# Optimization experiments

Hardware: AMD Instinct MI355X
Metric: run time of the kernel (lower is better)

The kernel has to match this reference:

```python
import jax, jax.numpy as jnp
import numpy as np

NUM_HEADS = 16


def setup_inputs() -> dict:
    key = jax.random.key(0)
    k1, k2, k3 = jax.random.split(key, 3)
    B, N, C = 8, 1024, 1024
    x = jax.random.normal(k1, (B, N, C), dtype=jnp.float32)
    w_qkv = jax.random.normal(k2, (3 * C, C), dtype=jnp.float32) * (C ** -0.5)
    w_proj = jax.random.normal(k3, (C, C), dtype=jnp.float32) * (C ** -0.5)
    b_proj = jnp.zeros((C,), dtype=jnp.float32)
    return {"x": x, "w_qkv": w_qkv, "w_proj": w_proj, "b_proj": b_proj}


def reference(x, w_qkv, w_proj, b_proj):
    B, N, C = x.shape
    H = NUM_HEADS
    d = C // H
    scale = d ** -0.5
    # qkv projection: (B, N, 3C) -> (3, B, H, N, d)
    qkv = jnp.einsum('bnc,oc->bno', x, w_qkv)
    qkv = qkv.reshape(B, N, 3, H, d).transpose(2, 0, 3, 1, 4)
    q, k, v = qkv[0], qkv[1], qkv[2]
    # spatial attention
    attn = jnp.einsum('bhnd,bhmd->bhnm', q, k) * scale
    attn = jax.nn.softmax(attn, axis=-1)
    out = jnp.einsum('bhnm,bhmd->bhnd', attn, v)
    out = out.transpose(0, 2, 1, 3).reshape(B, N, C)
    # output projection
    return jnp.einsum('bnc,oc->bno', out, w_proj) + b_proj
```

## Files before the change

### kernel.cpp

```cpp
#include <hip/hip_runtime.h>
#include <hip/hip_bf16.h>

typedef unsigned short u16;
typedef unsigned int u32;
typedef __bf16 bf16x8 __attribute__((ext_vector_type(8)));
typedef float f32x4 __attribute__((ext_vector_type(4)));

__device__ __forceinline__ u16 f2b(float f) {
    __bf16 h = (__bf16)f;
    return __builtin_bit_cast(u16, h);
}
__device__ __forceinline__ u32 f2b2(float lo, float hi) {
    return (u32)f2b(lo) | ((u32)f2b(hi) << 16);
}
__device__ __forceinline__ f32x4 mfma16(bf16x8 a, bf16x8 b, f32x4 c) {
    return __builtin_amdgcn_mfma_f32_16x16x32_bf16(a, b, c, 0, 0, 0);
}
__device__ __forceinline__ void async16(const u16* gsrc, u16* ldst) {
    __builtin_amdgcn_global_load_lds(
        (const __attribute__((address_space(1))) void*)gsrc,
        (__attribute__((address_space(3))) void*)ldst, 16, 0, 0);
}
__device__ __forceinline__ float exp2_raw(float x) {
#if __has_builtin(__builtin_amdgcn_exp2f)
    return __builtin_amdgcn_exp2f(x);
#else
    float r; asm("v_exp_f32 %0, %1" : "=v"(r) : "v"(x)); return r;
#endif
}

__global__ __launch_bounds__(256) void cvt_all(const float* __restrict__ x,
                                               const float* __restrict__ wq,
                                               const float* __restrict__ wp,
                                               u16* __restrict__ xb,
                                               u16* __restrict__ wqb,
                                               u16* __restrict__ wpb) {
    int i = (blockIdx.x * 256 + threadIdx.x) * 4;
    const float* src; u16* dst; int off; float scl;
    if (i < 8388608)       { src = x;  dst = xb;  off = i;            scl = 1.f; }
    else if (i < 9437184)  { src = wq; dst = wqb; off = i - 8388608;  scl = 0.18033688f; }
    else if (i < 11534336) { src = wq; dst = wqb; off = i - 8388608;  scl = 1.f; }
    else                   { src = wp; dst = wpb; off = i - 11534336; scl = 1.f; }
    float4 f = *(const float4*)(src + off);
    ushort4 o;
    o.x = f2b(f.x * scl); o.y = f2b(f.y * scl);
    o.z = f2b(f.z * scl); o.w = f2b(f.w * scl);
    *(ushort4*)(dst + off) = o;
}

template <bool F32OUT>
__device__ __forceinline__ void gemm_core(const u16* __restrict__ A,
                                          const u16* __restrict__ B,
                                          void* __restrict__ Cptr,
                                          const float* __restrict__ bias,
                                          int N, int K, int bm, int bn,
                                          u16* As, u16* Bs) {
    const int tid  = threadIdx.x;
    const int lane = tid & 63, wid = tid >> 6;
    const int quad = lane >> 4, l16 = lane & 15;
    const int wm = (wid >> 1) * 64, wn = (wid & 1) * 64;
    const int swr = l16 & 7;

    const int srow8  = lane >> 3;
    const int schunk = ((lane & 7) ^ srow8) << 3;

    const u16* Abase = A + (size_t)(bm * 128) * K;
    const u16* Bbase = B + (size_t)(bn * 128) * K;

    f32x4 acc[4][4] = {};

    for (int k0 = 0; k0 < K; k0 += 64) {
        __syncthreads();
#pragma unroll
        for (int j = 0; j < 4; ++j) {
            int rg = wid * 32 + j * 8;
            async16(Abase + (size_t)(rg + srow8) * K + k0 + schunk, &As[rg * 64]);
            async16(Bbase + (size_t)(rg + srow8) * K + k0 + schunk, &Bs[rg * 64]);
        }
        __syncthreads();
#pragma unroll
        for (int s = 0; s < 2; ++s) {
            bf16x8 af[4], bfr[4];
#pragma unroll
            for (int mt = 0; mt < 4; mt++) {
                int r = wm + mt * 16 + l16;
                af[mt] = *(const bf16x8*)&As[r * 64 + (((s * 4 + quad) ^ swr) << 3)];
            }
#pragma unroll
            for (int nt = 0; nt < 4; nt++) {
                int r = wn + nt * 16 + l16;
                bfr[nt] = *(const bf16x8*)&Bs[r * 64 + (((s * 4 + quad) ^ swr) << 3)];
            }
#pragma unroll
            for (int mt = 0; mt < 4; mt++)
#pragma unroll
                for (int nt = 0; nt < 4; nt++)
                    acc[mt][nt] = mfma16(af[mt], bfr[nt], acc[mt][nt]);
        }
    }
#pragma unroll
    for (int mt = 0; mt < 4; mt++) {
#pragma unroll
        for (int nt = 0; nt < 4; nt++) {
            int row = bm * 128 + wm + mt * 16 + quad * 4;
            int col = bn * 128 + wn + nt * 16 + l16;
            float bv = F32OUT ? bias[col] : 0.f;
#pragma unroll
            for (int r = 0; r < 4; r++) {
                if (F32OUT)
                    ((float*)Cptr)[(size_t)(row + r) * N + col] = acc[mt][nt][r] + bv;
                else
                    ((u16*)Cptr)[(size_t)(row + r) * N + col] = f2b(acc[mt][nt][r]);
            }
        }
    }
}

__global__ __launch_bounds__(256) void gemm_qkvt(const u16* __restrict__ xb,
                                                 const u16* __restrict__ wqkvb,
                                                 u16* __restrict__ qkb,
                                                 u16* __restrict__ vTb) {
    __shared__ u16 As[128 * 64];
    __shared__ u16 Bs[128 * 64];
    int id = blockIdx.x;
    if (id < 1024) {
        gemm_core<false>(xb, wqkvb, qkb, nullptr, 2048, 1024, id >> 4, id & 15, As, Bs);
    } else {
        int t = id - 1024;
        gemm_core<false>(wqkvb + (size_t)2048 * 1024, xb, vTb, nullptr,
                         8192, 1024, t >> 6, t & 63, As, Bs);
    }
}

__global__ __launch_bounds__(256) void gemm_proj(const u16* __restrict__ A,
                                                 const u16* __restrict__ B,
                                                 void* __restrict__ C,
                                                 const float* __restrict__ bias) {
    __shared__ u16 As[128 * 64];
    __shared__ u16 Bs[128 * 64];
    gemm_core<true>(A, B, C, bias, 1024, 1024, blockIdx.y, blockIdx.x, As, Bs);
}

__global__ __launch_bounds__(256, 5) void attn_kernel(const u16* __restrict__ qk,
                                                      const u16* __restrict__ vT,
                                                      u16* __restrict__ outb) {
    __shared__ u16 Ks[64 * 64];
    __shared__ u16 Vt[2][64 * 64];
    __shared__ u16 Ps[4 * 16 * 64];
    const int tid = threadIdx.x, lane = tid & 63, wid = tid >> 6;
    const int quad = lane >> 4, l16 = lane & 15;
    const int p = blockIdx.x;
    const int slot = p >> 3;
    const int bh = (p & 7) * 16 + (slot >> 4);
    const int qt = slot & 15;
    const int b = bh >> 4, h = bh & 15;
    const size_t base = (size_t)b * 1024;
    const int hoff = h * 64;

    const int sr_ = lane >> 3;
    const int sc_ = ((lane & 7) ^ sr_) * 8;
    const int sw = l16 & 7;

    const u16* qptr = qk + (base + qt * 64 + wid * 16 + l16) * 2048 + hoff + quad * 8;
    bf16x8 bq0 = *(const bf16x8*)qptr;
    bf16x8 bq1 = *(const bf16x8*)(qptr + 32);

    auto stageK = [&](int kt) {
#pragma unroll
        for (int j = 0; j < 2; ++j) {
            int rg = wid * 16 + j * 8;
            async16(qk + (base + kt * 64 + rg + sr_) * 2048 + 1024 + hoff + sc_,
                    &Ks[rg * 64]);
        }
    };
    auto stageV = [&](int kt, int bs) {
#pragma unroll
        for (int j = 0; j < 2; ++j) {
            int rg = wid * 16 + j * 8;
            async16(vT + (size_t)(hoff + rg + sr_) * 8192 + base + kt * 64 + sc_,
                    &Vt[bs][rg * 64]);
        }
    };

    f32x4 Oacc[4] = {};
    f32x4 lacc = {};
    bf16x8 vone;
#pragma unroll
    for (int i = 0; i < 8; ++i) vone[i] = (__bf16)1.0f;
    u16* Pw = &Ps[wid * (16 * 64)];
    bf16x8 ap0, ap1;

    stageK(0);
    asm volatile("s_waitcnt vmcnt(0)" ::: "memory");
    __builtin_amdgcn_s_barrier();
    __builtin_amdgcn_sched_barrier(0);

    for (int u = 0; u < 16; ++u) {
        const int cur = u & 1;

        f32x4 sacc[4] = {};
        __builtin_amdgcn_s_setprio(1);
#pragma unroll
        for (int nt = 0; nt < 4; nt++) {
            int row = nt * 16 + l16;
            bf16x8 ak0 = *(const bf16x8*)&Ks[row * 64 + ((quad ^ sw) << 3)];
            bf16x8 ak1 = *(const bf16x8*)&Ks[row * 64 + (((4 + quad) ^ sw) << 3)];
            sacc[nt] = mfma16(ak0, bq0, sacc[nt]);
            sacc[nt] = mfma16(ak1, bq1, sacc[nt]);
        }
        __builtin_amdgcn_s_setprio(0);

        __builtin_amdgcn_s_barrier();
        __builtin_amdgcn_sched_barrier(0);
        if (u < 15) stageK(u + 1);
        stageV(u, cur);

        if (u) {
            __builtin_amdgcn_s_setprio(1);
            lacc = mfma16(ap0, vone, lacc);
#pragma unroll
            for (int nv = 0; nv < 4; nv++) {
                int row = nv * 16 + l16;
                bf16x8 bv = *(const bf16x8*)&Vt[cur ^ 1][row * 64 + ((quad ^ sw) << 3)];
                Oacc[nv] = mfma16(ap0, bv, Oacc[nv]);
            }
            __builtin_amdgcn_s_setprio(0);
        }
#pragma unroll
        for (int nt = 0; nt < 2; nt++) {
            float p0 = exp2_raw(sacc[nt][0]);
            float p1 = exp2_raw(sacc[nt][1]);
            float p2 = exp2_raw(sacc[nt][2]);
            float p3 = exp2_raw(sacc[nt][3]);
            uint2 pk; pk.x = f2b2(p0, p1); pk.y = f2b2(p2, p3);
            *(uint2*)&Pw[l16 * 64 + (((nt * 2 + (quad >> 1)) ^ sw) << 3) + ((quad & 1) << 2)] = pk;
        }
        if (u) {
            __builtin_amdgcn_s_setprio(1);
            lacc = mfma16(ap1, vone, lacc);
#pragma unroll
            for (int nv = 0; nv < 4; nv++) {
                int row = nv * 16 + l16;
                bf16x8 bv = *(const bf16x8*)&Vt[cur ^ 1][row * 64 + (((4 + quad) ^ sw) << 3)];
                Oacc[nv] = mfma16(ap1, bv, Oacc[nv]);
            }
            __builtin_amdgcn_s_setprio(0);
        }
#pragma unroll
        for (int nt = 2; nt < 4; nt++) {
            float p0 = exp2_raw(sacc[nt][0]);
            float p1 = exp2_raw(sacc[nt][1]);
            float p2 = exp2_raw(sacc[nt][2]);
            float p3 = exp2_raw(sacc[nt][3]);
            uint2 pk; pk.x = f2b2(p0, p1); pk.y = f2b2(p2, p3);
            *(uint2*)&Pw[l16 * 64 + (((nt * 2 + (quad >> 1)) ^ sw) << 3) + ((quad & 1) << 2)] = pk;
        }

        asm volatile("s_waitcnt lgkmcnt(0)" ::: "memory");
        __builtin_amdgcn_wave_barrier();
        __builtin_amdgcn_sched_barrier(0);
        ap0 = *(const bf16x8*)&Pw[l16 * 64 + ((quad ^ sw) << 3)];
        ap1 = *(const bf16x8*)&Pw[l16 * 64 + (((4 + quad) ^ sw) << 3)];

        asm volatile("s_waitcnt vmcnt(0)" ::: "memory");
        __builtin_amdgcn_s_barrier();
        __builtin_amdgcn_sched_barrier(0);
    }

    __builtin_amdgcn_s_setprio(1);
    lacc = mfma16(ap0, vone, lacc);
#pragma unroll
    for (int nv = 0; nv < 4; nv++) {
        int row = nv * 16 + l16;
        bf16x8 bv = *(const bf16x8*)&Vt[1][row * 64 + ((quad ^ sw) << 3)];
        Oacc[nv] = mfma16(ap0, bv, Oacc[nv]);
    }
    lacc = mfma16(ap1, vone, lacc);
#pragma unroll
    for (int nv = 0; nv < 4; nv++) {
        int row = nv * 16 + l16;
        bf16x8 bv = *(const bf16x8*)&Vt[1][row * 64 + (((4 + quad) ^ sw) << 3)];
        Oacc[nv] = mfma16(ap1, bv, Oacc[nv]);
    }
    __builtin_amdgcn_s_setprio(0);

    float inv[4];
#pragma unroll
    for (int r = 0; r < 4; r++) inv[r] = 1.f / lacc[r];

#pragma unroll
    for (int nv = 0; nv < 4; nv++)
#pragma unroll
        for (int r = 0; r < 4; r++) {
            int row = qt * 64 + wid * 16 + quad * 4 + r;
            int col = hoff + nv * 16 + l16;
            outb[(base + row) * 1024 + col] = f2b(Oacc[nv][r] * inv[r]);
        }
}

extern "C" void kernel_launch(void* const* d_in, const int* in_sizes, int n_in,
                              void* d_out, int out_size, void* d_ws, size_t ws_size,
                              hipStream_t stream) {
    const float* x      = (const float*)d_in[0];
    const float* w_qkv  = (const float*)d_in[1];
    const float* w_proj = (const float*)d_in[2];
    const float* b_proj = (const float*)d_in[3];

    char* ws = (char*)d_ws;
    u16* xb     = (u16*)(ws);
    u16* wqkvb  = (u16*)(ws + 16777216);
    u16* wprojb = (u16*)(ws + 23068672);
    u16* qkb    = (u16*)(ws + 25165824);
    u16* vTb    = (u16*)(ws + 58720256);
    u16* attnb  = (u16*)(ws + 75497472);

    cvt_all<<<12288, 256, 0, stream>>>(x, w_qkv, w_proj, xb, wqkvb, wprojb);
    gemm_qkvt<<<1536, 256, 0, stream>>>(xb, wqkvb, qkb, vTb);
    attn_kernel<<<2048, 256, 0, stream>>>(qkb, vTb, attnb);
    gemm_proj<<<dim3(8, 64), 256, 0, stream>>>(attnb, wprojb, d_out, b_proj);
}
```

Measured before the change: 236.7 us.

## Replace QKV GEMM with 256x256 tile, 8-wave, double-buffered pipelined kernel

Swaps the 128x128 tile QKV/V^T projection GEMM for a new kernel that uses 256x256 output tiles with 8 waves per block. Global-to-LDS loads are double-buffered and interleaved with MFMA phases, using explicit barriers, vmcnt waits and setprio. The larger tile raises arithmetic intensity and the fine-grained schedule tries to overlap loads with compute. The costs are one block per CU with 64KB of LDS, a 384-block grid that may leave CUs partly idle on a 256-CU part, and higher register pressure.

```diff
diff --git a/kernel.cpp b/kernel.cpp
--- a/kernel.cpp
+++ b/kernel.cpp
@@ -48,6 +48,106 @@
     *(ushort4*)(dst + off) = o;
 }
 
+#define BARRIER_LG { __builtin_amdgcn_s_barrier(); \
+    asm volatile("s_waitcnt lgkmcnt(0)" ::: "memory"); \
+    __builtin_amdgcn_sched_barrier(0); }
+#define ENDBAR { __builtin_amdgcn_s_barrier(); __builtin_amdgcn_sched_barrier(0); }
+#define LDA(d_, s_) { _Pragma("unroll") for (int m = 0; m < 8; ++m) \
+    a[m][s_] = *(const bf16x8*)&As[d_][(wr*128 + m*16 + l16)*64 + (((s_*4+quad)^sw)<<3)]; }
+#define LDB(d_, nh_, s_) { \
+    b0 = *(const bf16x8*)&Bs[d_][(wc*64 + nh_*32 + l16)*64 + (((s_*4+quad)^sw)<<3)]; \
+    b1 = *(const bf16x8*)&Bs[d_][(wc*64 + nh_*32 + 16 + l16)*64 + (((s_*4+quad)^sw)<<3)]; }
+#define MM(nh_, s_) { __builtin_amdgcn_s_setprio(1); \
+    _Pragma("unroll") for (int m = 0; m < 8; ++m) { \
+        acc[m][nh_*2]   = mfma16(a[m][s_], b0, acc[m][nh_*2]); \
+        acc[m][nh_*2+1] = mfma16(a[m][s_], b1, acc[m][nh_*2+1]); } \
+    __builtin_amdgcn_s_setprio(0); }
+
+__global__ __launch_bounds__(512, 1) void gemm_qkvt8(const u16* __restrict__ xb,
+                                                     const u16* __restrict__ wqkvb,
+                                                     u16* __restrict__ qkb,
+                                                     u16* __restrict__ vTb) {
+    __shared__ u16 As[2][256 * 64];
+    __shared__ u16 Bs[2][256 * 64];
+    const int tid = threadIdx.x, lane = tid & 63, wid = tid >> 6;
+    const int quad = lane >> 4, l16 = lane & 15;
+    const int wr = wid >> 2, wc = wid & 3;
+    const int sw = l16 & 7;
+    const int sch = ((lane & 7) ^ (lane >> 3)) << 3;
+
+    const u16 *Abase, *Bbase; u16* Cp; int N, bm, bn;
+    const int id = blockIdx.x;
+    if (id < 256) {
+        Abase = xb; Bbase = wqkvb; Cp = qkb; N = 2048; bm = id >> 3; bn = id & 7;
+    } else {
+        int t2 = id - 256;
+        Abase = wqkvb + (size_t)2048 * 1024; Bbase = xb; Cp = vTb;
+        N = 8192; bm = t2 >> 5; bn = t2 & 31;
+    }
+    const int K = 1024;
+    Abase += (size_t)(bm * 256) * K;
+    Bbase += (size_t)(bn * 256) * K;
+
+    auto stA = [&](int tile, int h) {
+        if (tile >= 16) return;
+        const int d = tile & 1, k0 = tile << 6;
+#pragma unroll
+        for (int j = 0; j < 2; ++j) {
+            int rg = h * 128 + j * 64;
+            async16(Abase + (size_t)(rg + wid * 8 + (lane >> 3)) * K + k0 + sch,
+                    &As[d][(rg + wid * 8) * 64]);
+        }
+    };
+    auto stB = [&](int tile, int h) {
+        if (tile >= 16) return;
+        const int d = tile & 1, k0 = tile << 6;
+#pragma unroll
+        for (int j = 0; j < 2; ++j) {
+            int rg = h * 128 + j * 64;
+            async16(Bbase + (size_t)(rg + wid * 8 + (lane >> 3)) * K + k0 + sch,
+                    &Bs[d][(rg + wid * 8) * 64]);
+        }
+    };
+
+    f32x4 acc[8][4] = {};
+    bf16x8 a[8][2], b0, b1;
+
+    stA(0, 0); stA(0, 1); stB(0, 0); stB(0, 1); stA(1, 0); stA(1, 1);
+    asm volatile("s_waitcnt vmcnt(4)" ::: "memory");
+    __builtin_amdgcn_s_barrier();
+    __builtin_amdgcn_sched_barrier(0);
+
+    for (int J = 0; J < 8; ++J) {
+        const int t = 2 * J;
+        const bool last = (J == 7);
+        LDA(0, 0); LDB(0, 0, 0); stB(t + 1, 0); BARRIER_LG; MM(0, 0); ENDBAR;
+        LDA(0, 1); LDB(0, 1, 0); stB(t + 1, 1); BARRIER_LG; MM(1, 0); ENDBAR;
+        LDB(0, 0, 1); stA(t + 2, 0);            BARRIER_LG; MM(0, 1); ENDBAR;
+        LDB(0, 1, 1); stA(t + 2, 1);
+        if (last) asm volatile("s_waitcnt vmcnt(0)" ::: "memory");
+        else      asm volatile("s_waitcnt vmcnt(4)" ::: "memory");
+        BARRIER_LG; MM(1, 1); ENDBAR;
+        LDA(1, 0); LDB(1, 0, 0); stB(t + 2, 0); BARRIER_LG; MM(0, 0); ENDBAR;
+        LDA(1, 1); LDB(1, 1, 0); stB(t + 2, 1); BARRIER_LG; MM(1, 0); ENDBAR;
+        LDB(1, 0, 1); stA(t + 3, 0);            BARRIER_LG; MM(0, 1); ENDBAR;
+        LDB(1, 1, 1); stA(t + 3, 1);
+        if (last) asm volatile("s_waitcnt vmcnt(0)" ::: "memory");
+        else      asm volatile("s_waitcnt vmcnt(4)" ::: "memory");
+        BARRIER_LG; MM(1, 1); ENDBAR;
+    }
+
+#pragma unroll
+    for (int m = 0; m < 8; ++m)
+#pragma unroll
+        for (int j = 0; j < 4; ++j) {
+            int row = bm * 256 + wr * 128 + m * 16 + quad * 4;
+            int col = bn * 256 + wc * 64 + (j >> 1) * 32 + (j & 1) * 16 + l16;
+#pragma unroll
+            for (int r = 0; r < 4; ++r)
+                Cp[(size_t)(row + r) * N + col] = f2b(acc[m][j][r]);
+        }
+}
+
 template <bool F32OUT>
 __device__ __forceinline__ void gemm_core(const u16* __restrict__ A,
                                           const u16* __restrict__ B,
@@ -113,22 +213,6 @@
                     ((u16*)Cptr)[(size_t)(row + r) * N + col] = f2b(acc[mt][nt][r]);
             }
         }
-    }
-}
-
-__global__ __launch_bounds__(256) void gemm_qkvt(const u16* __restrict__ xb,
-                                                 const u16* __restrict__ wqkvb,
-                                                 u16* __restrict__ qkb,
-                                                 u16* __restrict__ vTb) {
-    __shared__ u16 As[128 * 64];
-    __shared__ u16 Bs[128 * 64];
-    int id = blockIdx.x;
-    if (id < 1024) {
-        gemm_core<false>(xb, wqkvb, qkb, nullptr, 2048, 1024, id >> 4, id & 15, As, Bs);
-    } else {
-        int t = id - 1024;
-        gemm_core<false>(wqkvb + (size_t)2048 * 1024, xb, vTb, nullptr,
-                         8192, 1024, t >> 6, t & 63, As, Bs);
     }
 }
 
@@ -315,7 +399,7 @@
     u16* attnb  = (u16*)(ws + 75497472);
 
     cvt_all<<<12288, 256, 0, stream>>>(x, w_qkv, w_proj, xb, wqkvb, wprojb);
-    gemm_qkvt<<<1536, 256, 0, stream>>>(xb, wqkvb, qkb, vTb);
+    gemm_qkvt8<<<384, 512, 0, stream>>>(xb, wqkvb, qkb, vTb);
     attn_kernel<<<2048, 256, 0, stream>>>(qkb, vTb, attnb);
     gemm_proj<<<dim3(8, 64), 256, 0, stream>>>(attnb, wprojb, d_out, b_proj);
 }
```

Result: slower. 245.8 us (+3.9%).
